# Kernel optimization log

Measured on AMD Instinct MI355X. Metric: run time of the kernel, lower is better.

Reference implementation:

```python
import jax, jax.numpy as jnp
import numpy as np

N_NODES = 100000
N_EDGES = 3200000
B = 64            # number of graphs / RNA batch
DIM = 16          # GINE hidden dim
NFP = 33          # protein node feature dim
EMB = 128         # embedding dim
MAXLEN = 3000     # rna_global length (conv1d in_channels)
LOCLEN = 2998     # rna_local length = 3000 - log4(64) + 1
NF = 32           # n_filters
KS = 8            # conv kernel size -> 128-8+1 = 121
FC_IN = NF * 121  # 3872
BN_EPS = 1e-5


def setup_inputs() -> dict:
    key = jax.random.key(0)
    ks = jax.random.split(key, 32)
    s = 0.1
    p = {}
    # forward data args
    p['pro_x'] = jax.random.normal(ks[0], (N_NODES, NFP), jnp.float32)
    p['pro_edge_index'] = jax.random.randint(ks[1], (2, N_EDGES), 0, N_NODES, jnp.int32)
    p['pro_weight'] = jax.random.uniform(ks[2], (N_EDGES, 1), jnp.float32)
    p['pro_batch'] = jnp.sort(jax.random.randint(ks[3], (N_NODES,), 0, B, jnp.int32))
    p['rna_global'] = jax.random.randint(ks[4], (B, MAXLEN), 0, 5, jnp.int32)
    p['rna_local'] = jax.random.randint(ks[5], (B, LOCLEN), 0, 65, jnp.int32)
    # GINE layer 1 (33 -> 16)
    p['g1_w1'] = jax.random.normal(ks[6], (NFP, DIM), jnp.float32) * s
    p['g1_b1'] = jnp.zeros((DIM,), jnp.float32)
    p['g1_w2'] = jax.random.normal(ks[7], (DIM, DIM), jnp.float32) * s
    p['g1_b2'] = jnp.zeros((DIM,), jnp.float32)
    p['g1_ew'] = jax.random.normal(ks[8], (1, NFP), jnp.float32) * s  # edge Linear(1, 33)
    p['g1_eb'] = jnp.zeros((NFP,), jnp.float32)
    p['g1_eps'] = jnp.zeros((), jnp.float32)
    # GINE layers 2-5 (16 -> 16), stacked on leading axis
    p['g_w1'] = jax.random.normal(ks[9], (4, DIM, DIM), jnp.float32) * s
    p['g_b1'] = jnp.zeros((4, DIM), jnp.float32)
    p['g_w2'] = jax.random.normal(ks[10], (4, DIM, DIM), jnp.float32) * s
    p['g_b2'] = jnp.zeros((4, DIM), jnp.float32)
    p['g_ew'] = jax.random.normal(ks[11], (4, 1, DIM), jnp.float32) * s  # edge Linear(1, 16)
    p['g_eb'] = jnp.zeros((4, DIM), jnp.float32)
    p['g_eps'] = jnp.zeros((4,), jnp.float32)
    # BatchNorm1d x5
    p['bn_gamma'] = jnp.ones((5, DIM), jnp.float32)
    p['bn_beta'] = jnp.zeros((5, DIM), jnp.float32)
    # fc1_xp (16 -> 128)
    p['fc1_xp_w'] = jax.random.normal(ks[12], (DIM, EMB), jnp.float32) * s
    p['fc1_xp_b'] = jnp.zeros((EMB,), jnp.float32)
    # RNA branch
    p['emb1'] = jax.random.normal(ks[13], (5, EMB), jnp.float32)
    p['emb2'] = jax.random.normal(ks[14], (65, EMB), jnp.float32)
    p['convr1_w'] = jax.random.normal(ks[15], (NF, MAXLEN, KS), jnp.float32) * 0.01
    p['convr1_b'] = jnp.zeros((NF,), jnp.float32)
    p['convr2_w'] = jax.random.normal(ks[16], (NF, LOCLEN, KS), jnp.float32) * 0.01
    p['convr2_b'] = jnp.zeros((NF,), jnp.float32)
    p['fcxr_w'] = jax.random.normal(ks[17], (FC_IN, EMB), jnp.float32) * 0.01
    p['fcxr_b'] = jnp.zeros((EMB,), jnp.float32)
    return p


def _gine(x, src, dst, ew, w1, b1, w2, b2, ew_w, ew_b, eps):
    # GINEConv: out = MLP((1+eps)*x + sum_j relu(x_j + edge_lin(e_ij)))
    e = ew @ ew_w + ew_b                       # [E, d]
    m = jax.nn.relu(x[src] + e)                # [E, d] gather + fuse
    agg = jax.ops.segment_sum(m, dst, num_segments=N_NODES)
    h = (1.0 + eps) * x + agg
    return jax.nn.relu(h @ w1 + b1) @ w2 + b2


def _bn(x, gamma, beta):
    mu = jnp.mean(x, axis=0)
    var = jnp.var(x, axis=0)
    return (x - mu) * jax.lax.rsqrt(var + BN_EPS) * gamma + beta


def _rna_branch(tokens, emb, cw, cb, fcw, fcb):
    x = emb[tokens]                            # [B, L, 128]
    y = jax.lax.conv_general_dilated(x, cw, (1,), 'VALID',
                                     dimension_numbers=('NCH', 'OIH', 'NCH'))
    y = y + cb[None, :, None]                  # [B, 32, 121]
    return y.reshape(y.shape[0], -1) @ fcw + fcb


def reference(pro_x, pro_edge_index, pro_weight, pro_batch, rna_global, rna_local,
              g1_w1, g1_b1, g1_w2, g1_b2, g1_ew, g1_eb, g1_eps,
              g_w1, g_b1, g_w2, g_b2, g_ew, g_eb, g_eps,
              bn_gamma, bn_beta, fc1_xp_w, fc1_xp_b,
              emb1, emb2, convr1_w, convr1_b, convr2_w, convr2_b, fcxr_w, fcxr_b):
    src, dst = pro_edge_index[0], pro_edge_index[1]
    # RNA global / local branches (shared fc_xr)
    xrg = _rna_branch(rna_global, emb1, convr1_w, convr1_b, fcxr_w, fcxr_b)
    xrl = _rna_branch(rna_local, emb2, convr2_w, convr2_b, fcxr_w, fcxr_b)
    # protein GINE stack
    xp = jax.nn.relu(_gine(pro_x, src, dst, pro_weight,
                           g1_w1, g1_b1, g1_w2, g1_b2, g1_ew, g1_eb, g1_eps))
    xp = _bn(xp, bn_gamma[0], bn_beta[0])
    for i in range(4):
        xp = jax.nn.relu(_gine(xp, src, dst, pro_weight,
                               g_w1[i], g_b1[i], g_w2[i], g_b2[i],
                               g_ew[i], g_eb[i], g_eps[i]))
        xp = _bn(xp, bn_gamma[i + 1], bn_beta[i + 1])
    # global mean pool over graphs
    sums = jax.ops.segment_sum(xp, pro_batch, num_segments=B)
    cnt = jax.ops.segment_sum(jnp.ones((N_NODES, 1), xp.dtype), pro_batch, num_segments=B)
    xp = jax.nn.relu((sums / jnp.maximum(cnt, 1.0)) @ fc1_xp_w + fc1_xp_b)
    # dropout in eval mode -> identity
    xc_rna = 0.5 * (xrg + xrl)
    return (xc_rna, xp)
```

## Files before the change

### kernel.cpp

```cpp
#include <hip/hip_runtime.h>
#include <hip/hip_fp16.h>

#define N_NODES 100000
#define N_EDGES 3200000
#define BGR 64
#define DIM 16
#define NFP 33
#define ROW1 32
#define H1STR 36
#define EMB 128
#define MAXLEN 3000
#define LOCLEN 2998
#define NF 32
#define KS 8
#define OUTT 121
#define FC_IN 3872
#define BN_EPSV 1e-5f
#define POOL_CHUNK 256
#define POOL_BLKS 391
#define MLPB 391
#define AGGB1 6250
#define AGGB16 3125
#define NBIN 391
#define BCNT_BLK 512
#define P1_CHUNK 4096
#define P1_BLOCKS 782
#define MAXBIN 9088
#define NKC 32
#define KCH 121
#define WDEC (1.f / 32767.f)
#define SEG_G 8

__global__ void __launch_bounds__(256) k_pre1(const int* __restrict__ dst,
                                              int* __restrict__ bh,
                                              const int* __restrict__ rg,
                                              const int* __restrict__ rl,
                                              int* __restrict__ blg, int* __restrict__ bpg,
                                              int* __restrict__ bll, int* __restrict__ bpl) {
    __shared__ int sh[NBIN];
    int t = threadIdx.x, bid = blockIdx.x;
    if (bid < BCNT_BLK) {
        for (int b = t; b < NBIN; b += 256) sh[b] = 0;
        __syncthreads();
        int e0 = bid * (N_EDGES / BCNT_BLK);
        int e1 = e0 + (N_EDGES / BCNT_BLK);
        for (int e = e0 + t; e < e1; e += 256) atomicAdd(&sh[dst[e] >> 8], 1);
        __syncthreads();
        for (int b = t; b < NBIN; b += 256) bh[b * BCNT_BLK + bid] = sh[b];
    } else {
        int idx = bid - BCNT_BLK;
        int which = idx >> 6, b = idx & 63;
        const int* tok = which ? rl : rg;
        int L = which ? LOCLEN : MAXLEN;
        int V = which ? 65 : 5;
        int* blist = which ? bll : blg;
        int* bptr = which ? bpl : bpg;
        int* hist = sh;
        int* cursor = sh + 70;
        if (t < V) hist[t] = 0;
        __syncthreads();
        for (int l = t; l < L; l += 256) atomicAdd(&hist[tok[b * L + l]], 1);
        __syncthreads();
        if (t == 0) {
            int run = 0;
            for (int v = 0; v < V; v++) {
                cursor[v] = run;
                bptr[b * (V + 1) + v] = run;
                run += hist[v];
            }
            bptr[b * (V + 1) + V] = run;
        }
        __syncthreads();
        for (int l = t; l < L; l += 256) {
            int v = tok[b * L + l];
            int p = atomicAdd(&cursor[v], 1);
            blist[b * L + p] = l;
        }
    }
}

__global__ void __launch_bounds__(512) k_binscan(const int* __restrict__ bh,
                                                 int* __restrict__ binoff,
                                                 int* __restrict__ bincur) {
    __shared__ int sc[512];
    int t = threadIdx.x;
    int s = 0;
    if (t < NBIN) {
        const int4* row = (const int4*)(bh + t * BCNT_BLK);
        #pragma unroll 4
        for (int k = 0; k < BCNT_BLK / 4; k++) {
            int4 v = row[k];
            s += v.x + v.y + v.z + v.w;
        }
    }
    sc[t] = s;
    __syncthreads();
    for (int off = 1; off < 512; off <<= 1) {
        int v = (t >= off) ? sc[t - off] : 0;
        __syncthreads();
        sc[t] += v;
        __syncthreads();
    }
    int excl = sc[t] - s;
    if (t <= NBIN) binoff[t] = excl;
    if (t < NBIN) bincur[t] = excl;
}

__global__ void __launch_bounds__(256) k_part1(const int* __restrict__ src,
                                               const int* __restrict__ dst,
                                               const float* __restrict__ w,
                                               int* __restrict__ bincur,
                                               int2* __restrict__ tmp_sw) {
    __shared__ int2 srec[P1_CHUNK];
    __shared__ unsigned short sbin[P1_CHUNK];
    __shared__ unsigned short sperm[P1_CHUNK];
    __shared__ int hist[NBIN];
    __shared__ int off[NBIN];
    __shared__ int cur[NBIN];
    __shared__ int base[NBIN];
    __shared__ int sc[512];
    int t = threadIdx.x;
    int g0 = blockIdx.x * P1_CHUNK;
    int cn = N_EDGES - g0; if (cn > P1_CHUNK) cn = P1_CHUNK;
    for (int b = t; b < NBIN; b += 256) hist[b] = 0;
    __syncthreads();
    for (int j = t; j < cn; j += 256) {
        int d = dst[g0 + j];
        int b = d >> 8;
        sbin[j] = (unsigned short)b;
        srec[j] = make_int2(src[g0 + j] | ((d & 255) << 20), __float_as_int(w[g0 + j]));
        atomicAdd(&hist[b], 1);
    }
    __syncthreads();
    sc[t] = (t < NBIN) ? hist[t] : 0;
    sc[256 + t] = (256 + t < NBIN) ? hist[256 + t] : 0;
    __syncthreads();
    for (int o = 1; o <= 256; o <<= 1) {
        int v0 = (t >= o) ? sc[t - o] : 0;
        int v1 = sc[256 + t - o];
        __syncthreads();
        sc[t] += v0;
        sc[256 + t] += v1;
        __syncthreads();
    }
    for (int b = t; b < NBIN; b += 256) {
        int e = sc[b] - hist[b];
        off[b] = e;
        cur[b] = e;
        int c = hist[b];
        base[b] = c ? atomicAdd(&bincur[b], c) : 0;
    }
    __syncthreads();
    for (int j = t; j < cn; j += 256) {
        int p = atomicAdd(&cur[sbin[j]], 1);
        sperm[p] = (unsigned short)j;
    }
    __syncthreads();
    for (int p = t; p < cn; p += 256) {
        int j = sperm[p];
        int b = sbin[j];
        tmp_sw[base[b] + (p - off[b])] = srec[j];
    }
}

__global__ void __launch_bounds__(256) k_part2(const int2* __restrict__ tmp_sw,
                                               const int* __restrict__ binoff,
                                               unsigned* __restrict__ er,
                                               int* __restrict__ ptr) {
    __shared__ unsigned char sdl[MAXBIN];
    __shared__ unsigned short perm[MAXBIN];
    __shared__ int hist[256];
    __shared__ int cur[256];
    __shared__ int sc[256];
    int t = threadIdx.x, b = blockIdx.x;
    int nlo = b << 8;
    int e0 = binoff[b], e1 = binoff[b + 1];
    int cnt = e1 - e0;
    int stage = cnt < MAXBIN ? cnt : MAXBIN;
    hist[t] = 0;
    __syncthreads();
    for (int j = t; j < stage; j += 256) {
        unsigned char dl = (unsigned char)((tmp_sw[e0 + j].x >> 20) & 255);
        sdl[j] = dl;
        atomicAdd(&hist[dl], 1);
    }
    for (int j = stage + t; j < cnt; j += 256)
        atomicAdd(&hist[(tmp_sw[e0 + j].x >> 20) & 255], 1);
    __syncthreads();
    int v = hist[t];
    sc[t] = v;
    __syncthreads();
    for (int off = 1; off < 256; off <<= 1) {
        int u = (t >= off) ? sc[t - off] : 0;
        __syncthreads();
        sc[t] += u;
        __syncthreads();
    }
    int excl = sc[t] - v;
    cur[t] = excl;
    if (nlo + t < N_NODES) ptr[nlo + t] = e0 + excl;
    if (b == NBIN - 1 && t == 0) ptr[N_NODES] = N_EDGES;
    __syncthreads();
    for (int j = t; j < stage; j += 256) {
        int p = atomicAdd(&cur[sdl[j]], 1);
        perm[p] = (unsigned short)j;
    }
    __syncthreads();
    for (int j = stage + t; j < cnt; j += 256) {
        int2 sw = tmp_sw[e0 + j];
        int p = atomicAdd(&cur[(sw.x >> 20) & 255], 1);
        unsigned wq = (unsigned)(__int_as_float(sw.y) * 32767.f + 0.5f);
        er[e0 + p] = ((unsigned)sw.x & 0x1FFFFu) | (wq << 17);
    }
    for (int p = t; p < stage; p += 256) {
        int2 sw = tmp_sw[e0 + perm[p]];
        unsigned wq = (unsigned)(__int_as_float(sw.y) * 32767.f + 0.5f);
        er[e0 + p] = ((unsigned)sw.x & 0x1FFFFu) | (wq << 17);
    }
}

__global__ void __launch_bounds__(256) k_pre2(const float* __restrict__ cw1,
                                              const float* __restrict__ cw2,
                                              float* __restrict__ cwTg,
                                              float* __restrict__ cwTl,
                                              const float* __restrict__ x,
                                              __half* __restrict__ xh,
                                              __half* __restrict__ xh32) {
    int bid = blockIdx.x, t = threadIdx.x;
    if (bid < MAXLEN) {
        cwTg[bid * 256 + t] = cw1[(t >> 3) * (MAXLEN * KS) + bid * KS + (t & 7)];
    } else if (bid < MAXLEN + LOCLEN) {
        int ll = bid - MAXLEN;
        cwTl[ll * 256 + t] = cw2[(t >> 3) * (LOCLEN * KS) + ll * KS + (t & 7)];
    } else {
        int i = (bid - (MAXLEN + LOCLEN)) * 256 + t;
        if (i < N_NODES * NFP) {
            int n = i / NFP, f = i - n * NFP;
            __half v = __float2half(x[i]);
            if (f < 32) xh[n * ROW1 + f] = v;
            else xh32[n] = v;
        }
    }
}

__device__ __forceinline__ void acc8p(float a[8], uint4 r, float wv,
                                      const float* __restrict__ ewf,
                                      const float* __restrict__ ebf) {
    float2 f01 = __half22float2(*(__half2*)&r.x);
    float2 f23 = __half22float2(*(__half2*)&r.y);
    float2 f45 = __half22float2(*(__half2*)&r.z);
    float2 f67 = __half22float2(*(__half2*)&r.w);
    float x[8] = {f01.x, f01.y, f23.x, f23.y, f45.x, f45.y, f67.x, f67.y};
    #pragma unroll
    for (int j = 0; j < 8; j++)
        a[j] += fmaxf(x[j] + fmaf(wv, ewf[j], ebf[j]), 0.f);
}

__device__ __forceinline__ void acc8s(float a[8], uint4 r, float wv,
                                      const float* __restrict__ scf,
                                      const float* __restrict__ cbf,
                                      const float* __restrict__ ewf) {
    float2 f01 = __half22float2(*(__half2*)&r.x);
    float2 f23 = __half22float2(*(__half2*)&r.y);
    float2 f45 = __half22float2(*(__half2*)&r.z);
    float2 f67 = __half22float2(*(__half2*)&r.w);
    float x[8] = {f01.x, f01.y, f23.x, f23.y, f45.x, f45.y, f67.x, f67.y};
    #pragma unroll
    for (int j = 0; j < 8; j++)
        a[j] += fmaxf(fmaf(x[j], scf[j], fmaf(wv, ewf[j], cbf[j])), 0.f);
}

__global__ void __launch_bounds__(256) k_agg1(
    const __half* __restrict__ xh, const __half* __restrict__ xh32,
    const int* __restrict__ ptr, const unsigned* __restrict__ er,
    const float* __restrict__ ew, const float* __restrict__ ebv,
    const float* __restrict__ epsp, float* __restrict__ h) {
    int t = threadIdx.x;
    int wave = t >> 6, lane = t & 63;
    int nl = lane >> 4;
    int slot = (lane >> 2) & 3;
    int q = lane & 3;
    float ewf[8], ebf[8];
    #pragma unroll
    for (int j = 0; j < 8; j++) { ewf[j] = ew[q * 8 + j]; ebf[j] = ebv[q * 8 + j]; }
    float ew32 = ew[32], eb32 = ebv[32];
    float ep = 1.f + epsp[0];
    int node = blockIdx.x * 16 + wave * 4 + nl;
    int e0 = ptr[node], e1 = ptr[node + 1];
    float a[8] = {0, 0, 0, 0, 0, 0, 0, 0};
    float a32 = 0.f;
    int i = e0 + slot;
    while (i + 4 < e1) {
        unsigned ev0 = er[i];
        unsigned ev1 = er[i + 4];
        int s0 = ev0 & 0x1FFFF, s1 = ev1 & 0x1FFFF;
        float wv0 = (float)(ev0 >> 17) * WDEC;
        float wv1 = (float)(ev1 >> 17) * WDEC;
        uint4 r0 = *(const uint4*)(xh + s0 * ROW1 + q * 8);
        uint4 r1 = *(const uint4*)(xh + s1 * ROW1 + q * 8);
        acc8p(a, r0, wv0, ewf, ebf);
        acc8p(a, r1, wv1, ewf, ebf);
        if (q == 0) {
            a32 += fmaxf(__half2float(xh32[s0]) + fmaf(wv0, ew32, eb32), 0.f);
            a32 += fmaxf(__half2float(xh32[s1]) + fmaf(wv1, ew32, eb32), 0.f);
        }
        i += 8;
    }
    if (i < e1) {
        unsigned ev = er[i];
        int s = ev & 0x1FFFF;
        float wv = (float)(ev >> 17) * WDEC;
        uint4 r = *(const uint4*)(xh + s * ROW1 + q * 8);
        acc8p(a, r, wv, ewf, ebf);
        if (q == 0)
            a32 += fmaxf(__half2float(xh32[s]) + fmaf(wv, ew32, eb32), 0.f);
    }
    #pragma unroll
    for (int j = 0; j < 8; j++) {
        a[j] += __shfl_xor(a[j], 4);
        a[j] += __shfl_xor(a[j], 8);
    }
    a32 += __shfl_xor(a32, 4);
    a32 += __shfl_xor(a32, 8);
    if (slot == 0) {
        uint4 sraw = *(const uint4*)(xh + node * ROW1 + q * 8);
        float2 s01 = __half22float2(*(__half2*)&sraw.x);
        float2 s23 = __half22float2(*(__half2*)&sraw.y);
        float2 s45 = __half22float2(*(__half2*)&sraw.z);
        float2 s67 = __half22float2(*(__half2*)&sraw.w);
        float* hp = h + node * H1STR + q * 8;
        *(float4*)hp = make_float4(ep * s01.x + a[0], ep * s01.y + a[1],
                                   ep * s23.x + a[2], ep * s23.y + a[3]);
        *(float4*)(hp + 4) = make_float4(ep * s45.x + a[4], ep * s45.y + a[5],
                                         ep * s67.x + a[6], ep * s67.y + a[7]);
        if (q == 0)
            h[node * H1STR + 32] = ep * __half2float(xh32[node]) + a32;
    }
}

__global__ void __launch_bounds__(256) k_agg16(
    const __half* __restrict__ zh, const int* __restrict__ ptr,
    const unsigned* __restrict__ er,
    const float* __restrict__ ew, const float* __restrict__ ebv,
    const float* __restrict__ epsp,
    const float* __restrict__ bnstat, const float* __restrict__ gamma,
    const float* __restrict__ beta, float* __restrict__ h) {
    int t = threadIdx.x;
    int wave = t >> 6, lane = t & 63;
    int nl = lane >> 3;
    int slot = (lane >> 1) & 3;
    int hh = lane & 1;
    float ep = 1.f + epsp[0];
    const float invn = 1.f / (float)N_NODES;
    float scf[8], shf[8], cbf[8], ewf[8];
    #pragma unroll
    for (int j = 0; j < 8; j++) {
        int f = hh * 8 + j;
        float mu = bnstat[f] * invn;
        float var = bnstat[DIM + f] * invn - mu * mu;
        float sc = gamma[f] * rsqrtf(var + BN_EPSV);
        scf[j] = sc;
        shf[j] = beta[f] - mu * sc;
        cbf[j] = shf[j] + ebv[f];
        ewf[j] = ew[f];
    }
    int node = blockIdx.x * 32 + wave * 8 + nl;
    int e0 = ptr[node], e1 = ptr[node + 1];
    float a[8] = {0, 0, 0, 0, 0, 0, 0, 0};
    int i = e0 + slot;
    while (i + 4 < e1) {
        unsigned ev0 = er[i];
        unsigned ev1 = er[i + 4];
        float wv0 = (float)(ev0 >> 17) * WDEC;
        float wv1 = (float)(ev1 >> 17) * WDEC;
        uint4 r0 = *(const uint4*)(zh + (ev0 & 0x1FFFFu) * DIM + hh * 8);
        uint4 r1 = *(const uint4*)(zh + (ev1 & 0x1FFFFu) * DIM + hh * 8);
        acc8s(a, r0, wv0, scf, cbf, ewf);
        acc8s(a, r1, wv1, scf, cbf, ewf);
        i += 8;
    }
    if (i < e1) {
        unsigned ev = er[i];
        float wv = (float)(ev >> 17) * WDEC;
        uint4 r = *(const uint4*)(zh + (ev & 0x1FFFFu) * DIM + hh * 8);
        acc8s(a, r, wv, scf, cbf, ewf);
    }
    #pragma unroll
    for (int j = 0; j < 8; j++) a[j] += __shfl_xor(a[j], 2);
    #pragma unroll
    for (int j = 0; j < 8; j++) a[j] += __shfl_xor(a[j], 4);
    if (slot == 0) {
        uint4 sraw = *(const uint4*)(zh + node * DIM + hh * 8);
        float2 s01 = __half22float2(*(__half2*)&sraw.x);
        float2 s23 = __half22float2(*(__half2*)&sraw.y);
        float2 s45 = __half22float2(*(__half2*)&sraw.z);
        float2 s67 = __half22float2(*(__half2*)&sraw.w);
        float xs[8] = {s01.x, s01.y, s23.x, s23.y, s45.x, s45.y, s67.x, s67.y};
        float o8[8];
        #pragma unroll
        for (int j = 0; j < 8; j++)
            o8[j] = ep * fmaf(xs[j], scf[j], shf[j]) + a[j];
        float* hp = h + node * DIM + hh * 8;
        *(float4*)hp = make_float4(o8[0], o8[1], o8[2], o8[3]);
        *(float4*)(hp + 4) = make_float4(o8[4], o8[5], o8[6], o8[7]);
    }
}

__device__ __forceinline__ void mlp_bn_tail(float zv[16], bool active, int t,
                                            float* __restrict__ bnstat) {
    __shared__ float red[4][32];
    float zs[16], zq[16];
    #pragma unroll
    for (int o = 0; o < 16; o++) {
        zs[o] = active ? zv[o] : 0.f;
        zq[o] = active ? zv[o] * zv[o] : 0.f;
    }
    #pragma unroll
    for (int m = 1; m <= 32; m <<= 1) {
        #pragma unroll
        for (int o = 0; o < 16; o++) {
            zs[o] += __shfl_xor(zs[o], m);
            zq[o] += __shfl_xor(zq[o], m);
        }
    }
    int wave = t >> 6, lane = t & 63;
    if (lane == 0) {
        #pragma unroll
        for (int o = 0; o < 16; o++) {
            red[wave][o] = zs[o];
            red[wave][16 + o] = zq[o];
        }
    }
    __syncthreads();
    if (t < 32)
        atomicAdd(&bnstat[t], red[0][t] + red[1][t] + red[2][t] + red[3][t]);
}

__device__ __forceinline__ void store_zh(__half* __restrict__ zh, int n, float zv[16]) {
    __half2 p[8];
    #pragma unroll
    for (int j = 0; j < 8; j++) p[j] = __floats2half2_rn(zv[2 * j], zv[2 * j + 1]);
    *(uint4*)(zh + n * DIM) = *(uint4*)&p[0];
    *(uint4*)(zh + n * DIM + 8) = *(uint4*)&p[4];
}

__global__ void __launch_bounds__(256) k_mlp16(
    const float* __restrict__ h,
    const float* __restrict__ W1, const float* __restrict__ b1,
    const float* __restrict__ W2, const float* __restrict__ b2,
    __half* __restrict__ zh, float* __restrict__ bnstat) {
    __shared__ float W1s[256], W2s[256], b1s[16], b2s[16];
    int t = threadIdx.x;
    W1s[t] = W1[t];
    W2s[t] = W2[t];
    if (t < 16) { b1s[t] = b1[t]; b2s[t] = b2[t]; }
    __syncthreads();
    int n = blockIdx.x * 256 + t;
    bool active = n < N_NODES;
    float zv[16];
    if (active) {
        float hv[16];
        #pragma unroll
        for (int j = 0; j < 4; j++) {
            float4 v = *(const float4*)(h + n * DIM + j * 4);
            hv[j * 4] = v.x; hv[j * 4 + 1] = v.y; hv[j * 4 + 2] = v.z; hv[j * 4 + 3] = v.w;
        }
        float tv[16];
        #pragma unroll
        for (int o = 0; o < 16; o++) {
            float s = b1s[o];
            #pragma unroll
            for (int f = 0; f < 16; f++) s += hv[f] * W1s[f * 16 + o];
            tv[o] = fmaxf(s, 0.f);
        }
        #pragma unroll
        for (int o = 0; o < 16; o++) {
            float s = b2s[o];
            #pragma unroll
            for (int f = 0; f < 16; f++) s += tv[f] * W2s[f * 16 + o];
            zv[o] = fmaxf(s, 0.f);
        }
        store_zh(zh, n, zv);
    }
    mlp_bn_tail(zv, active, t, bnstat);
}

__global__ void __launch_bounds__(256) k_mlp1(
    const float* __restrict__ h,
    const float* __restrict__ W1, const float* __restrict__ b1,
    const float* __restrict__ W2, const float* __restrict__ b2,
    __half* __restrict__ zh, float* __restrict__ bnstat) {
    __shared__ float W1s[NFP * 16], W2s[256], b1s[16], b2s[16];
    int t = threadIdx.x;
    for (int j = t; j < NFP * 16; j += 256) W1s[j] = W1[j];
    W2s[t] = W2[t];
    if (t < 16) { b1s[t] = b1[t]; b2s[t] = b2[t]; }
    __syncthreads();
    int n = blockIdx.x * 256 + t;
    bool active = n < N_NODES;
    float zv[16];
    if (active) {
        float hv[NFP];
        #pragma unroll
        for (int j = 0; j < 8; j++) {
            float4 v = *(const float4*)(h + n * H1STR + j * 4);
            hv[j * 4] = v.x; hv[j * 4 + 1] = v.y; hv[j * 4 + 2] = v.z; hv[j * 4 + 3] = v.w;
        }
        hv[32] = h[n * H1STR + 32];
        float tv[16];
        #pragma unroll
        for (int o = 0; o < 16; o++) {
            float s = b1s[o];
            #pragma unroll
            for (int f = 0; f < NFP; f++) s += hv[f] * W1s[f * 16 + o];
            tv[o] = fmaxf(s, 0.f);
        }
        #pragma unroll
        for (int o = 0; o < 16; o++) {
            float s = b2s[o];
            #pragma unroll
            for (int f = 0; f < 16; f++) s += tv[f] * W2s[f * 16 + o];
            zv[o] = fmaxf(s, 0.f);
        }
        store_zh(zh, n, zv);
    }
    mlp_bn_tail(zv, active, t, bnstat);
}

__global__ void __launch_bounds__(256) k_pool(const __half* __restrict__ zh,
                                              const int* __restrict__ batch,
                                              const float* __restrict__ bnstat,
                                              const float* __restrict__ gamma,
                                              const float* __restrict__ beta,
                                              float* __restrict__ gsum,
                                              float* __restrict__ gcnt) {
    __shared__ float lsum[BGR * DIM];
    __shared__ float lcnt[BGR];
    int t = threadIdx.x;
    for (int j = t; j < BGR * DIM; j += 256) lsum[j] = 0.f;
    if (t < BGR) lcnt[t] = 0.f;
    __syncthreads();
    int f = t & 15, r = t >> 4;
    const float invn = 1.f / (float)N_NODES;
    float mu = bnstat[f] * invn;
    float var = bnstat[DIM + f] * invn - mu * mu;
    float sc = gamma[f] * rsqrtf(var + BN_EPSV);
    float sh = beta[f] - mu * sc;
    int start = blockIdx.x * POOL_CHUNK;
    float acc = 0.f, cacc = 0.f;
    int cur = -1;
    for (int i = 0; i < POOL_CHUNK / 16; i++) {
        int n = start + r + i * 16;
        if (n >= N_NODES) break;
        int b = batch[n];
        if (b != cur) {
            if (cur >= 0) {
                atomicAdd(&lsum[cur * DIM + f], acc);
                if (f == 0) atomicAdd(&lcnt[cur], cacc);
            }
            cur = b; acc = 0.f; cacc = 0.f;
        }
        acc += fmaf(__half2float(zh[n * DIM + f]), sc, sh);
        cacc += 1.f;
    }
    if (cur >= 0) {
        atomicAdd(&lsum[cur * DIM + f], acc);
        if (f == 0) atomicAdd(&lcnt[cur], cacc);
    }
    __syncthreads();
    for (int j = t; j < BGR * DIM; j += 256) {
        float v = lsum[j];
        if (v != 0.f) atomicAdd(&gsum[j], v);
    }
    if (t < BGR) {
        float v = lcnt[t];
        if (v != 0.f) atomicAdd(&gcnt[t], v);
    }
}

__global__ void __launch_bounds__(256) k_wsum(const int* __restrict__ blg,
                                              const int* __restrict__ bpg,
                                              const int* __restrict__ bll,
                                              const int* __restrict__ bpl,
                                              const float* __restrict__ cwTg,
                                              const float* __restrict__ cwTl,
                                              float* __restrict__ Wp,
                                              float* __restrict__ Wlocal) {
    int b = blockIdx.x, y = blockIdx.y;
    int t = threadIdx.x;
    if (y < 40) {
        int v = y >> 3, seg = y & 7;
        int s = bpg[b * 6 + v], e = bpg[b * 6 + v + 1];
        int cnt = e - s;
        int chunk = (cnt + SEG_G - 1) / SEG_G;
        int j0 = s + seg * chunk;
        int j1 = j0 + chunk; if (j1 > e) j1 = e;
        const int* bl = blg + b * MAXLEN;
        float acc = 0.f;
        int j = j0;
        while (j + 3 < j1) {
            int t0 = bl[j], t1 = bl[j + 1], t2 = bl[j + 2], t3 = bl[j + 3];
            float a0 = cwTg[t0 * 256 + t];
            float a1 = cwTg[t1 * 256 + t];
            float a2 = cwTg[t2 * 256 + t];
            float a3 = cwTg[t3 * 256 + t];
            acc += a0 + a1 + a2 + a3;
            j += 4;
        }
        while (j < j1) {
            acc += cwTg[bl[j] * 256 + t];
            j++;
        }
        Wp[((b * 5 + v) * SEG_G + seg) * 256 + t] = acc;
    } else {
        int v = y - 40;
        int s = bpl[b * 66 + v], e = bpl[b * 66 + v + 1];
        const int* bl = bll + b * LOCLEN;
        float acc = 0.f;
        int j = s;
        while (j + 3 < e) {
            int t0 = bl[j], t1 = bl[j + 1], t2 = bl[j + 2], t3 = bl[j + 3];
            float a0 = cwTl[t0 * 256 + t];
            float a1 = cwTl[t1 * 256 + t];
            float a2 = cwTl[t2 * 256 + t];
            float a3 = cwTl[t3 * 256 + t];
            acc += a0 + a1 + a2 + a3;
            j += 4;
        }
        while (j < e) {
            acc += cwTl[bl[j] * 256 + t];
            j++;
        }
        int o = t >> 3, k = t & 7;
        Wlocal[((b * NF + o) * 65 + v) * KS + k] = acc;
    }
}

__global__ void __launch_bounds__(128) k_yfc(const float* __restrict__ Wpg,
                                             const float* __restrict__ Wl,
                                             const float* __restrict__ emb1,
                                             const float* __restrict__ emb2,
                                             const float* __restrict__ cb1,
                                             const float* __restrict__ cb2,
                                             const float* __restrict__ w,
                                             float* __restrict__ partial) {
    int which = blockIdx.y;
    int bo = blockIdx.x;
    int b = bo >> 5, o = bo & 31;
    int t = threadIdx.x;
    const float* emb = which ? emb2 : emb1;
    const float* cb = which ? cb2 : cb1;
    int V = which ? 65 : 5;
    __shared__ float Wsh[65 * KS];
    __shared__ float ych[OUTT];
    if (which) {
        const float* Wrow = Wl + (b * NF + o) * 65 * KS;
        for (int j = t; j < 65 * KS; j += 128) Wsh[j] = Wrow[j];
    } else {
        for (int j = t; j < 5 * KS; j += 128) {
            int v = j >> 3, k = j & 7;
            const float* p = Wpg + (b * 5 + v) * SEG_G * 256 + o * 8 + k;
            float s = 0.f;
            #pragma unroll
            for (int g = 0; g < SEG_G; g++) s += p[g * 256];
            Wsh[j] = s;
        }
    }
    __syncthreads();
    if (t < OUTT) {
        float acc = cb[o];
        for (int v = 0; v < V; v++) {
            const float* ep = emb + v * EMB + t;
            #pragma unroll
            for (int k = 0; k < KS; k++) acc += Wsh[v * KS + k] * ep[k];
        }
        ych[t] = acc;
    }
    __syncthreads();
    float facc = 0.f;
    const float* wp = w + (o * OUTT) * EMB + t;
    #pragma unroll 4
    for (int jj = 0; jj < OUTT; jj++) facc += ych[jj] * wp[jj * EMB];
    partial[((which * BGR + b) * NKC + o) * EMB + t] = facc;
}

__global__ void __launch_bounds__(128) k_tail(const float* __restrict__ partial,
                                              const float* __restrict__ bias,
                                              const float* __restrict__ gsum,
                                              const float* __restrict__ gcnt,
                                              const float* __restrict__ w,
                                              const float* __restrict__ xpb,
                                              float* __restrict__ out) {
    int b = blockIdx.x;
    int e = threadIdx.x;
    if (blockIdx.y == 0) {
        const float* pg = partial + b * NKC * EMB + e;
        const float* pl = partial + (BGR + b) * NKC * EMB + e;
        float ag = bias[e], al = bias[e];
        #pragma unroll
        for (int k = 0; k < NKC; k++) { ag += pg[k * EMB]; al += pl[k * EMB]; }
        out[b * EMB + e] = 0.5f * (ag + al);
    } else {
        float inv = 1.f / fmaxf(gcnt[b], 1.f);
        float acc = xpb[e];
        #pragma unroll
        for (int f = 0; f < DIM; f++) acc += gsum[b * DIM + f] * inv * w[f * EMB + e];
        out[BGR * EMB + b * EMB + e] = fmaxf(acc, 0.f);
    }
}

extern "C" void kernel_launch(void* const* d_in, const int* in_sizes, int n_in,
                              void* d_out, int out_size, void* d_ws, size_t ws_size,
                              hipStream_t stream) {
    const float* pro_x = (const float*)d_in[0];
    const int* eidx = (const int*)d_in[1];
    const int* esrc = eidx;
    const int* edst = eidx + N_EDGES;
    const float* pw = (const float*)d_in[2];
    const int* batch = (const int*)d_in[3];
    const int* rg = (const int*)d_in[4];
    const int* rl = (const int*)d_in[5];
    const float* g1_w1 = (const float*)d_in[6];
    const float* g1_b1 = (const float*)d_in[7];
    const float* g1_w2 = (const float*)d_in[8];
    const float* g1_b2 = (const float*)d_in[9];
    const float* g1_ew = (const float*)d_in[10];
    const float* g1_eb = (const float*)d_in[11];
    const float* g1_eps = (const float*)d_in[12];
    const float* g_w1 = (const float*)d_in[13];
    const float* g_b1 = (const float*)d_in[14];
    const float* g_w2 = (const float*)d_in[15];
    const float* g_b2 = (const float*)d_in[16];
    const float* g_ew = (const float*)d_in[17];
    const float* g_eb = (const float*)d_in[18];
    const float* g_eps = (const float*)d_in[19];
    const float* bn_gamma = (const float*)d_in[20];
    const float* bn_beta = (const float*)d_in[21];
    const float* fc1_xp_w = (const float*)d_in[22];
    const float* fc1_xp_b = (const float*)d_in[23];
    const float* emb1 = (const float*)d_in[24];
    const float* emb2 = (const float*)d_in[25];
    const float* convr1_w = (const float*)d_in[26];
    const float* convr1_b = (const float*)d_in[27];
    const float* convr2_w = (const float*)d_in[28];
    const float* convr2_b = (const float*)d_in[29];
    const float* fcxr_w = (const float*)d_in[30];
    const float* fcxr_b = (const float*)d_in[31];
    float* out = (float*)d_out;

    float* wsf = (float*)d_ws;
    int* ptr       = (int*)wsf;        wsf += 100128;
    int* binoff    = (int*)wsf;        wsf += 512;
    int* bincur    = (int*)wsf;        wsf += 512;
    unsigned* er   = (unsigned*)wsf;   wsf += 2 * N_EDGES;
    float* stats   = wsf;              wsf += 1280;
    float* un = wsf;
    int2* tmp_sw = (int2*)un;
    int* bh      = (int*)(un + 7200000);
    float* cwTg  = un;
    float* cwTl  = un + 768000;
    __half* zh   = (__half*)(un + 1600000);
    __half* xh1  = (__half*)(un + 2400000);
    __half* xh32 = (__half*)(un + 4000000);
    float* Wpg   = un + 4300000;
    float* Wl    = un + 5000000;
    int* blg     = (int*)(un + 6600000);
    int* bll     = (int*)(un + 6800000);
    int* bpg     = (int*)(un + 7000000);
    int* bpl     = (int*)(un + 7001000);
    float* fcpart = un + 6600000;
    float* h      = un + 7400000;
    float* gsum   = stats;
    float* gcnt   = stats + 1024;
    float* bnstat = stats + 1088;

    hipMemsetAsync(stats, 0, 1280 * sizeof(float), stream);

    k_pre1<<<BCNT_BLK + 128, 256, 0, stream>>>(edst, bh, rg, rl, blg, bpg, bll, bpl);
    k_binscan<<<1, 512, 0, stream>>>(bh, binoff, bincur);
    k_part1<<<P1_BLOCKS, 256, 0, stream>>>(esrc, edst, pw, bincur, tmp_sw);
    k_part2<<<NBIN, 256, 0, stream>>>(tmp_sw, binoff, er, ptr);

    k_pre2<<<MAXLEN + LOCLEN + (N_NODES * NFP + 255) / 256, 256, 0, stream>>>(
        convr1_w, convr2_w, cwTg, cwTl, pro_x, xh1, xh32);

    k_wsum<<<dim3(BGR, 105), 256, 0, stream>>>(blg, bpg, bll, bpl, cwTg, cwTl, Wpg, Wl);
    k_yfc<<<dim3(BGR * NF, 2), 128, 0, stream>>>(Wpg, Wl, emb1, emb2, convr1_b, convr2_b,
                                                 fcxr_w, fcpart);

    k_agg1<<<AGGB1, 256, 0, stream>>>(xh1, xh32, ptr, er, g1_ew, g1_eb, g1_eps, h);
    k_mlp1<<<MLPB, 256, 0, stream>>>(h, g1_w1, g1_b1, g1_w2, g1_b2, zh, bnstat);
    for (int i = 0; i < 4; i++) {
        k_agg16<<<AGGB16, 256, 0, stream>>>(zh, ptr, er,
                                            g_ew + i * DIM, g_eb + i * DIM, g_eps + i,
                                            bnstat + i * 32, bn_gamma + i * DIM,
                                            bn_beta + i * DIM, h);
        k_mlp16<<<MLPB, 256, 0, stream>>>(h, g_w1 + i * DIM * DIM, g_b1 + i * DIM,
                                          g_w2 + i * DIM * DIM, g_b2 + i * DIM, zh,
                                          bnstat + (i + 1) * 32);
    }
    k_pool<<<POOL_BLKS, 256, 0, stream>>>(zh, batch, bnstat + 4 * 32,
                                          bn_gamma + 4 * DIM, bn_beta + 4 * DIM, gsum, gcnt);
    k_tail<<<dim3(BGR, 2), 128, 0, stream>>>(fcpart, fcxr_b, gsum, gcnt,
                                             fc1_xp_w, fc1_xp_b, out);
}
```

Before: 560.9 us.

## Split layer-1 aggregation into two passes by source-node half for cache locality

The CSR partition step now sorts each node's edges by destination and also by whether the source index falls in the lower or upper half of the node range, and records a mid pointer per node. Layer-1 aggregation is split into two kernels: the first gathers only lower-half sources and the second only upper-half sources, adding onto the partial result. Each pass then gathers from a half-size slice of the 33-wide feature table, which is meant to fit better in L2 and cut random-gather misses. The cost is an extra kernel launch, a second read-modify-write of h, a wider histogram in the partition kernel, and the ptrm buffer reusing the bh workspace region.

```diff
diff --git a/kernel.cpp b/kernel.cpp
--- a/kernel.cpp
+++ b/kernel.cpp
@@ -26,6 +26,7 @@
 #define P1_CHUNK 4096
 #define P1_BLOCKS 782
 #define MAXBIN 9088
+#define SRC_MID 50000
 #define NKC 32
 #define KCH 121
 #define WDEC (1.f / 32767.f)
@@ -166,39 +167,52 @@
 __global__ void __launch_bounds__(256) k_part2(const int2* __restrict__ tmp_sw,
                                                const int* __restrict__ binoff,
                                                unsigned* __restrict__ er,
-                                               int* __restrict__ ptr) {
-    __shared__ unsigned char sdl[MAXBIN];
+                                               int* __restrict__ ptr,
+                                               int* __restrict__ ptrm) {
+    __shared__ unsigned short sdl[MAXBIN];
     __shared__ unsigned short perm[MAXBIN];
-    __shared__ int hist[256];
-    __shared__ int cur[256];
-    __shared__ int sc[256];
+    __shared__ int hist[512];
+    __shared__ int cur[512];
+    __shared__ int sc[512];
     int t = threadIdx.x, b = blockIdx.x;
     int nlo = b << 8;
     int e0 = binoff[b], e1 = binoff[b + 1];
     int cnt = e1 - e0;
     int stage = cnt < MAXBIN ? cnt : MAXBIN;
     hist[t] = 0;
+    hist[256 + t] = 0;
     __syncthreads();
     for (int j = t; j < stage; j += 256) {
-        unsigned char dl = (unsigned char)((tmp_sw[e0 + j].x >> 20) & 255);
-        sdl[j] = dl;
-        atomicAdd(&hist[dl], 1);
-    }
-    for (int j = stage + t; j < cnt; j += 256)
-        atomicAdd(&hist[(tmp_sw[e0 + j].x >> 20) & 255], 1);
-    __syncthreads();
-    int v = hist[t];
-    sc[t] = v;
-    __syncthreads();
-    for (int off = 1; off < 256; off <<= 1) {
-        int u = (t >= off) ? sc[t - off] : 0;
-        __syncthreads();
-        sc[t] += u;
-        __syncthreads();
-    }
-    int excl = sc[t] - v;
-    cur[t] = excl;
-    if (nlo + t < N_NODES) ptr[nlo + t] = e0 + excl;
+        int x = tmp_sw[e0 + j].x;
+        int key = (((x >> 20) & 255) << 1) | ((x & 0x1FFFF) >= SRC_MID ? 1 : 0);
+        sdl[j] = (unsigned short)key;
+        atomicAdd(&hist[key], 1);
+    }
+    for (int j = stage + t; j < cnt; j += 256) {
+        int x = tmp_sw[e0 + j].x;
+        int key = (((x >> 20) & 255) << 1) | ((x & 0x1FFFF) >= SRC_MID ? 1 : 0);
+        atomicAdd(&hist[key], 1);
+    }
+    __syncthreads();
+    int v0 = hist[t], v1 = hist[256 + t];
+    sc[t] = v0;
+    sc[256 + t] = v1;
+    __syncthreads();
+    for (int o = 1; o <= 256; o <<= 1) {
+        int u0 = (t >= o) ? sc[t - o] : 0;
+        int u1 = sc[256 + t - o];
+        __syncthreads();
+        sc[t] += u0;
+        sc[256 + t] += u1;
+        __syncthreads();
+    }
+    cur[t] = sc[t] - v0;
+    cur[256 + t] = sc[256 + t] - v1;
+    __syncthreads();
+    if (nlo + t < N_NODES) {
+        ptr[nlo + t] = e0 + sc[2 * t] - hist[2 * t];
+        ptrm[nlo + t] = e0 + sc[2 * t + 1] - hist[2 * t + 1];
+    }
     if (b == NBIN - 1 && t == 0) ptr[N_NODES] = N_EDGES;
     __syncthreads();
     for (int j = t; j < stage; j += 256) {
@@ -208,7 +222,8 @@
     __syncthreads();
     for (int j = stage + t; j < cnt; j += 256) {
         int2 sw = tmp_sw[e0 + j];
-        int p = atomicAdd(&cur[(sw.x >> 20) & 255], 1);
+        int key = (((sw.x >> 20) & 255) << 1) | ((sw.x & 0x1FFFF) >= SRC_MID ? 1 : 0);
+        int p = atomicAdd(&cur[key], 1);
         unsigned wq = (unsigned)(__int_as_float(sw.y) * 32767.f + 0.5f);
         er[e0 + p] = ((unsigned)sw.x & 0x1FFFFu) | (wq << 17);
     }
@@ -270,11 +285,12 @@
         a[j] += fmaxf(fmaf(x[j], scf[j], fmaf(wv, ewf[j], cbf[j])), 0.f);
 }
 
-__global__ void __launch_bounds__(256) k_agg1(
+__global__ void __launch_bounds__(256) k_agg1a(
     const __half* __restrict__ xh, const __half* __restrict__ xh32,
-    const int* __restrict__ ptr, const unsigned* __restrict__ er,
+    const int* __restrict__ ptr, const int* __restrict__ ptrm,
+    const unsigned* __restrict__ er,
     const float* __restrict__ ew, const float* __restrict__ ebv,
-    const float* __restrict__ epsp, float* __restrict__ h) {
+    float* __restrict__ h) {
     int t = threadIdx.x;
     int wave = t >> 6, lane = t & 63;
     int nl = lane >> 4;
@@ -284,9 +300,8 @@
     #pragma unroll
     for (int j = 0; j < 8; j++) { ewf[j] = ew[q * 8 + j]; ebf[j] = ebv[q * 8 + j]; }
     float ew32 = ew[32], eb32 = ebv[32];
-    float ep = 1.f + epsp[0];
     int node = blockIdx.x * 16 + wave * 4 + nl;
-    int e0 = ptr[node], e1 = ptr[node + 1];
+    int e0 = ptr[node], e1 = ptrm[node];
     float a[8] = {0, 0, 0, 0, 0, 0, 0, 0};
     float a32 = 0.f;
     int i = e0 + slot;
@@ -323,18 +338,82 @@
     a32 += __shfl_xor(a32, 4);
     a32 += __shfl_xor(a32, 8);
     if (slot == 0) {
+        float* hp = h + node * H1STR + q * 8;
+        *(float4*)hp = make_float4(a[0], a[1], a[2], a[3]);
+        *(float4*)(hp + 4) = make_float4(a[4], a[5], a[6], a[7]);
+        if (q == 0)
+            h[node * H1STR + 32] = a32;
+    }
+}
+
+__global__ void __launch_bounds__(256) k_agg1b(
+    const __half* __restrict__ xh, const __half* __restrict__ xh32,
+    const int* __restrict__ ptr, const int* __restrict__ ptrm,
+    const unsigned* __restrict__ er,
+    const float* __restrict__ ew, const float* __restrict__ ebv,
+    const float* __restrict__ epsp, float* __restrict__ h) {
+    int t = threadIdx.x;
+    int wave = t >> 6, lane = t & 63;
+    int nl = lane >> 4;
+    int slot = (lane >> 2) & 3;
+    int q = lane & 3;
+    float ewf[8], ebf[8];
+    #pragma unroll
+    for (int j = 0; j < 8; j++) { ewf[j] = ew[q * 8 + j]; ebf[j] = ebv[q * 8 + j]; }
+    float ew32 = ew[32], eb32 = ebv[32];
+    float ep = 1.f + epsp[0];
+    int node = blockIdx.x * 16 + wave * 4 + nl;
+    int e0 = ptrm[node], e1 = ptr[node + 1];
+    float a[8] = {0, 0, 0, 0, 0, 0, 0, 0};
+    float a32 = 0.f;
+    int i = e0 + slot;
+    while (i + 4 < e1) {
+        unsigned ev0 = er[i];
+        unsigned ev1 = er[i + 4];
+        int s0 = ev0 & 0x1FFFF, s1 = ev1 & 0x1FFFF;
+        float wv0 = (float)(ev0 >> 17) * WDEC;
+        float wv1 = (float)(ev1 >> 17) * WDEC;
+        uint4 r0 = *(const uint4*)(xh + s0 * ROW1 + q * 8);
+        uint4 r1 = *(const uint4*)(xh + s1 * ROW1 + q * 8);
+        acc8p(a, r0, wv0, ewf, ebf);
+        acc8p(a, r1, wv1, ewf, ebf);
+        if (q == 0) {
+            a32 += fmaxf(__half2float(xh32[s0]) + fmaf(wv0, ew32, eb32), 0.f);
+            a32 += fmaxf(__half2float(xh32[s1]) + fmaf(wv1, ew32, eb32), 0.f);
+        }
+        i += 8;
+    }
+    if (i < e1) {
+        unsigned ev = er[i];
+        int s = ev & 0x1FFFF;
+        float wv = (float)(ev >> 17) * WDEC;
+        uint4 r = *(const uint4*)(xh + s * ROW1 + q * 8);
+        acc8p(a, r, wv, ewf, ebf);
+        if (q == 0)
+            a32 += fmaxf(__half2float(xh32[s]) + fmaf(wv, ew32, eb32), 0.f);
+    }
+    #pragma unroll
+    for (int j = 0; j < 8; j++) {
+        a[j] += __shfl_xor(a[j], 4);
+        a[j] += __shfl_xor(a[j], 8);
+    }
+    a32 += __shfl_xor(a32, 4);
+    a32 += __shfl_xor(a32, 8);
+    if (slot == 0) {
+        float* hp = h + node * H1STR + q * 8;
+        float4 p0 = *(float4*)hp;
+        float4 p1 = *(float4*)(hp + 4);
         uint4 sraw = *(const uint4*)(xh + node * ROW1 + q * 8);
         float2 s01 = __half22float2(*(__half2*)&sraw.x);
         float2 s23 = __half22float2(*(__half2*)&sraw.y);
         float2 s45 = __half22float2(*(__half2*)&sraw.z);
         float2 s67 = __half22float2(*(__half2*)&sraw.w);
-        float* hp = h + node * H1STR + q * 8;
-        *(float4*)hp = make_float4(ep * s01.x + a[0], ep * s01.y + a[1],
-                                   ep * s23.x + a[2], ep * s23.y + a[3]);
-        *(float4*)(hp + 4) = make_float4(ep * s45.x + a[4], ep * s45.y + a[5],
-                                         ep * s67.x + a[6], ep * s67.y + a[7]);
+        *(float4*)hp = make_float4(ep * s01.x + a[0] + p0.x, ep * s01.y + a[1] + p0.y,
+                                   ep * s23.x + a[2] + p0.z, ep * s23.y + a[3] + p0.w);
+        *(float4*)(hp + 4) = make_float4(ep * s45.x + a[4] + p1.x, ep * s45.y + a[5] + p1.y,
+                                         ep * s67.x + a[6] + p1.z, ep * s67.y + a[7] + p1.w);
         if (q == 0)
-            h[node * H1STR + 32] = ep * __half2float(xh32[node]) + a32;
+            h[node * H1STR + 32] = ep * __half2float(xh32[node]) + a32 + h[node * H1STR + 32];
     }
 }
 
@@ -757,6 +836,7 @@
     float* un = wsf;
     int2* tmp_sw = (int2*)un;
     int* bh      = (int*)(un + 7200000);
+    int* ptrm    = (int*)(un + 7200000);
     float* cwTg  = un;
     float* cwTl  = un + 768000;
     __half* zh   = (__half*)(un + 1600000);
@@ -779,7 +859,7 @@
     k_pre1<<<BCNT_BLK + 128, 256, 0, stream>>>(edst, bh, rg, rl, blg, bpg, bll, bpl);
     k_binscan<<<1, 512, 0, stream>>>(bh, binoff, bincur);
     k_part1<<<P1_BLOCKS, 256, 0, stream>>>(esrc, edst, pw, bincur, tmp_sw);
-    k_part2<<<NBIN, 256, 0, stream>>>(tmp_sw, binoff, er, ptr);
+    k_part2<<<NBIN, 256, 0, stream>>>(tmp_sw, binoff, er, ptr, ptrm);
 
     k_pre2<<<MAXLEN + LOCLEN + (N_NODES * NFP + 255) / 256, 256, 0, stream>>>(
         convr1_w, convr2_w, cwTg, cwTl, pro_x, xh1, xh32);
@@ -788,7 +868,8 @@
     k_yfc<<<dim3(BGR * NF, 2), 128, 0, stream>>>(Wpg, Wl, emb1, emb2, convr1_b, convr2_b,
                                                  fcxr_w, fcpart);
 
-    k_agg1<<<AGGB1, 256, 0, stream>>>(xh1, xh32, ptr, er, g1_ew, g1_eb, g1_eps, h);
+    k_agg1a<<<AGGB1, 256, 0, stream>>>(xh1, xh32, ptr, ptrm, er, g1_ew, g1_eb, h);
+    k_agg1b<<<AGGB1, 256, 0, stream>>>(xh1, xh32, ptr, ptrm, er, g1_ew, g1_eb, g1_eps, h);
     k_mlp1<<<MLPB, 256, 0, stream>>>(h, g1_w1, g1_b1, g1_w2, g1_b2, zh, bnstat);
     for (int i = 0; i < 4; i++) {
         k_agg16<<<AGGB16, 256, 0, stream>>>(zh, ptr, er,
```

Result: no change. 566.6 us (+1.0%).
